# Performance work log

Measured on AMD Instinct MI355X. Metric: run time of the kernel, lower is better.

## Reference

```python
import jax, jax.numpy as jnp
import numpy as np

B, N, D = 1, 4096, 320
HEADS, DIM_HEAD = 8, 40
PHASE, Hm, Wm = 3, 64, 64  # guidance mask spatial dims; Hm*Wm == N


def setup_inputs() -> dict:
    key = jax.random.key(0)
    ks = jax.random.split(key, 7)
    s = 0.02
    x = jax.random.normal(ks[0], (B, N, D), jnp.float32)
    guidance_mask = jax.random.bernoulli(ks[1], 0.25, (B, PHASE, Hm, Wm)).astype(jnp.float32)
    Wq = jax.random.normal(ks[2], (D, HEADS * DIM_HEAD), jnp.float32) * s
    Wk = jax.random.normal(ks[3], (D, HEADS * DIM_HEAD), jnp.float32) * s
    Wv = jax.random.normal(ks[4], (D, HEADS * DIM_HEAD), jnp.float32) * s
    Wo = jax.random.normal(ks[5], (HEADS * DIM_HEAD, D), jnp.float32) * s
    bo = jnp.zeros((D,), jnp.float32)
    return {"x": x, "guidance_mask": guidance_mask, "Wq": Wq, "Wk": Wk,
            "Wv": Wv, "Wo": Wo, "bo": bo}


def reference(x, guidance_mask, Wq, Wk, Wv, Wo, bo):
    b, n, _ = x.shape
    h, dh = HEADS, DIM_HEAD
    scale = dh ** (-0.5)

    def split_heads(t):
        # b n (h d) -> (b h) n d
        return t.reshape(b, n, h, dh).transpose(0, 2, 1, 3).reshape(b * h, n, dh)

    q = split_heads(x @ Wq)
    k = split_heads(x @ Wk)
    v = split_heads(x @ Wv)

    sim = jnp.einsum('bid,bjd->bij', q, k) * scale  # (b*h, n, n)

    _, p, Hh, Ww = guidance_mask.shape
    HW = Hh * Ww  # == n
    g = guidance_mask.reshape(b, p, HW)
    # sum over phases of outer products, clamped at 1 (binary block mask)
    mask_sim = jnp.minimum(jnp.einsum('bpi,bpj->bij', g, g), 1.0)  # (b, HW, HW)
    mask_sim = jnp.repeat(mask_sim, h, axis=0)  # (b*h, HW, HW), heads within each b

    neg = -jnp.finfo(sim.dtype).max
    # original: sim[:, :, :HW][mask_sim == 0] = -max ; here n == HW so full matrix
    sim = jnp.where(mask_sim == 0, neg, sim)

    attn = jax.nn.softmax(sim, axis=-1)
    out = jnp.einsum('bij,bjd->bid', attn, v)  # (b*h, n, dh)
    out = out.reshape(b, h, n, dh).transpose(0, 2, 1, 3).reshape(b, n, h * dh)
    return out @ Wo + bo
```

## Files before the change

### kernel.cpp

```cpp
#include <hip/hip_runtime.h>
#include <hip/hip_bf16.h>
#include <stdint.h>

#define NT 4096
#define DM 320
#define NH 8
#define DH 40
#define QSCALE 0.22811013f
#define PSTR 68
#define KFJB 640

typedef float f32x4 __attribute__((ext_vector_type(4)));
typedef __bf16 bf16x8 __attribute__((ext_vector_type(8)));

__device__ __forceinline__ unsigned short f2b(float f) {
  unsigned u = __builtin_bit_cast(unsigned, f);
  u += 0x7FFFu + ((u >> 16) & 1u);
  return (unsigned short)(u >> 16);
}

__device__ __forceinline__ bf16x8 ld_bf8(const unsigned short* p) {
  uint4 v = *(const uint4*)p;
  return __builtin_bit_cast(bf16x8, v);
}

__device__ __forceinline__ f32x4 mfma16(bf16x8 a, bf16x8 b, f32x4 c) {
  return __builtin_amdgcn_mfma_f32_16x16x32_bf16(a, b, c, 0, 0, 0);
}

__device__ __forceinline__ float fexp2(float x) {
#if __has_builtin(__builtin_amdgcn_exp2f)
  return __builtin_amdgcn_exp2f(x);
#else
  float r; asm("v_exp_f32 %0, %1" : "=v"(r) : "v"(x)); return r;
#endif
}

__device__ __forceinline__ uint2 pack4(float a, float b, float c, float d) {
  uint2 pk;
  pk.x = (unsigned)f2b(a) | ((unsigned)f2b(b) << 16);
  pk.y = (unsigned)f2b(c) | ((unsigned)f2b(d) << 16);
  return pk;
}

__device__ __forceinline__ uint4 idfrag(int idx) {
  uint4 r;
  r.x = (idx == 0 ? 0x3F80u : 0u) | (idx == 1 ? 0x3F800000u : 0u);
  r.y = (idx == 2 ? 0x3F80u : 0u) | (idx == 3 ? 0x3F800000u : 0u);
  r.z = (idx == 4 ? 0x3F80u : 0u) | (idx == 5 ? 0x3F800000u : 0u);
  r.w = (idx == 6 ? 0x3F80u : 0u) | (idx == 7 ? 0x3F800000u : 0u);
  return r;
}

__device__ __forceinline__ size_t fmi(int tile, int nk, int k, int o) {
  return ((size_t)tile * nk + (k >> 5)) * 512 + (size_t)((k >> 3) & 3) * 128 +
         (size_t)(o & 15) * 8 + (k & 7);
}

__global__ __launch_bounds__(256) void prep_kernel(
    const float* __restrict__ x, const float* __restrict__ g,
    const float* __restrict__ Wq, const float* __restrict__ Wk,
    const float* __restrict__ Wv, const float* __restrict__ Wo,
    unsigned short* __restrict__ xbf, unsigned char* __restrict__ sgp,
    unsigned short* __restrict__ Wtf, int* __restrict__ perm,
    int* __restrict__ invp, int* __restrict__ nqp,
    unsigned char* __restrict__ tsig) {
  const int b = blockIdx.x, t = threadIdx.x;
  if (b == 100) {
    __shared__ unsigned long long sa[256], sb[256];
    unsigned char mys[16];
    unsigned long long ca = 0ull, cb = 0ull;
#pragma unroll
    for (int i = 0; i < 16; ++i) {
      int tok = t * 16 + i;
      unsigned s = 0;
      if (g[tok] != 0.f)          s |= 1u;
      if (g[NT + tok] != 0.f)     s |= 2u;
      if (g[2 * NT + tok] != 0.f) s |= 4u;
      mys[i] = (unsigned char)s;
      if (s < 4) ca += 1ull << (16 * s);
      else       cb += 1ull << (16 * (s - 4));
    }
    sa[t] = ca; sb[t] = cb;
    __syncthreads();
    for (int off = 1; off < 256; off <<= 1) {
      unsigned long long va = (t >= off) ? sa[t - off] : 0ull;
      unsigned long long vb = (t >= off) ? sb[t - off] : 0ull;
      __syncthreads();
      sa[t] += va; sb[t] += vb;
      __syncthreads();
    }
    const unsigned long long ta = sa[255], tb = sb[255];
    const int t1 = (int)((ta >> 16) & 0xffff), t2 = (int)((ta >> 32) & 0xffff),
              t3 = (int)((ta >> 48) & 0xffff), t4 = (int)(tb & 0xffff),
              t5 = (int)((tb >> 16) & 0xffff), t6 = (int)((tb >> 32) & 0xffff),
              t7 = (int)((tb >> 48) & 0xffff);
    const int b1 = 0, b2 = t1, b3 = b2 + t2, b4 = b3 + t3, b5 = b4 + t4,
              b6 = b5 + t5, b7 = b6 + t6, b0 = b7 + t7;
    unsigned long long ra = sa[t] - ca;
    unsigned long long rb = sb[t] - cb;
    ra += ((unsigned long long)(unsigned)b0)        |
          ((unsigned long long)(unsigned)b1 << 16)  |
          ((unsigned long long)(unsigned)b2 << 32)  |
          ((unsigned long long)(unsigned)b3 << 48);
    rb += ((unsigned long long)(unsigned)b4)        |
          ((unsigned long long)(unsigned)b5 << 16)  |
          ((unsigned long long)(unsigned)b6 << 32)  |
          ((unsigned long long)(unsigned)b7 << 48);
#pragma unroll
    for (int i = 0; i < 16; ++i) {
      int tok = t * 16 + i;
      unsigned s = mys[i];
      int sh = 16 * (int)(s & 3u);
      int p;
      if (s < 4) { p = (int)((ra >> sh) & 0xffff); ra += 1ull << sh; }
      else       { p = (int)((rb >> sh) & 0xffff); rb += 1ull << sh; }
      perm[p] = tok; invp[tok] = p; sgp[p] = (unsigned char)s;
    }
    if (t == 0) nqp[0] = b0;
    if (t < 64) {
      const int lo = t * 64, hi = lo + 64;
      unsigned o = 0;
      if (b1 < hi && b2 > lo && b2 > b1) o |= 1u;
      if (b2 < hi && b3 > lo && b3 > b2) o |= 2u;
      if (b3 < hi && b4 > lo && b4 > b3) o |= 3u;
      if (b4 < hi && b5 > lo && b5 > b4) o |= 4u;
      if (b5 < hi && b6 > lo && b6 > b5) o |= 5u;
      if (b6 < hi && b7 > lo && b7 > b6) o |= 6u;
      if (b7 < hi && b0 > lo && b0 > b7) o |= 7u;
      tsig[t] = (unsigned char)o;
    }
    return;
  }
  if (b > 100) {
    int base = (b - 101) * 2560;
#pragma unroll
    for (int j = 0; j < 10; ++j) {
      int i = (base + j * 256 + t) * 4;
      int m = i / DM, k = i % DM;
      float4 v = *(const float4*)(x + i);
      ushort4 u;
      u.x = f2b(v.x); u.y = f2b(v.y); u.z = f2b(v.z); u.w = f2b(v.w);
      *(ushort4*)(xbf + fmi(m >> 4, 10, k, m)) = u;
    }
    return;
  }
  __shared__ __align__(16) unsigned short lt[64 * 72];
  int kx = b % 5, cy = b / 5;
  int cm = cy % 5;
  const float* src;
  int rowbase;
  if (cy < 5)       { src = Wq; rowbase = cm * 64; }
  else if (cy < 10) { src = Wk; rowbase = 320 + cm * 64; }
  else if (cy < 15) { src = Wv; rowbase = 640 + cm * 64; }
  else              { src = Wo; rowbase = 960 + cm * 64; }
  const int c0 = cm * 64;
  const int k0 = kx * 64;
#pragma unroll
  for (int i = 0; i < 4; ++i) {
    int kr = (t >> 4) + i * 16, cc = (t & 15) * 4;
    float4 w4 = *(const float4*)&src[(size_t)(k0 + kr) * DM + c0 + cc];
    lt[(cc + 0) * 72 + kr] = f2b(w4.x);
    lt[(cc + 1) * 72 + kr] = f2b(w4.y);
    lt[(cc + 2) * 72 + kr] = f2b(w4.z);
    lt[(cc + 3) * 72 + kr] = f2b(w4.w);
  }
  __syncthreads();
#pragma unroll
  for (int i = 0; i < 2; ++i) {
    int idx = t + i * 256, cl = idx >> 3, ch = idx & 7;
    int c = rowbase + cl, k = k0 + ch * 8;
    *(uint4*)&Wtf[fmi(c >> 4, 10, k, c)] = *(const uint4*)&lt[cl * 72 + ch * 8];
  }
}

__global__ __launch_bounds__(256, 4) void qkv_gemm(
    const unsigned short* __restrict__ xbf, const unsigned short* __restrict__ Wtf,
    const int* __restrict__ invp,
    unsigned short* __restrict__ Qb, unsigned short* __restrict__ Kf,
    unsigned short* __restrict__ Vk) {
  const int t = threadIdx.x;
  const int w = t >> 6, lane = t & 63, quad = lane >> 4, ln = lane & 15;
  const int m0 = blockIdx.x * 64;
  const int cy = blockIdx.y;
  const int a = cy / 5;
  const int cc0 = (cy % 5) * 64;
  const int mt = (m0 >> 4) + w;
  const int ct0 = a * 20 + (cc0 >> 4);

  f32x4 acc[4] = {{0,0,0,0},{0,0,0,0},{0,0,0,0},{0,0,0,0}};
  for (int kc = 0; kc < 10; ++kc) {
    bf16x8 xf = ld_bf8(xbf + ((size_t)(mt * 10 + kc)) * 512 + lane * 8);
#pragma unroll
    for (int nt = 0; nt < 4; ++nt) {
      bf16x8 wf = ld_bf8(Wtf + ((size_t)((ct0 + nt) * 10 + kc)) * 512 + lane * 8);
      acc[nt] = mfma16(wf, xf, acc[nt]);
    }
  }
  const int bp = invp[m0 + w * 16 + ln];
  if (a == 0) {
#pragma unroll
    for (int nt = 0; nt < 4; ++nt) {
      int c = cc0 + nt * 16 + quad * 4;
      int h = c / DH, d = c % DH;
      uint2 pk = pack4(acc[nt][0] * QSCALE, acc[nt][1] * QSCALE,
                       acc[nt][2] * QSCALE, acc[nt][3] * QSCALE);
      *(uint2*)&Qb[((size_t)h * NT + bp) * 64 + d] = pk;
    }
  } else {
    unsigned short* dst = (a == 1) ? Kf : Vk;
#pragma unroll
    for (int nt = 0; nt < 4; ++nt) {
      int c = cc0 + nt * 16 + quad * 4;
      int h = c / DH, d = c % DH;
      uint2 pk = pack4(acc[nt][0], acc[nt][1], acc[nt][2], acc[nt][3]);
      size_t base = ((size_t)h * 256 + (bp >> 4)) * KFJB;
      size_t idx = (d < 32)
          ? base + (size_t)(d >> 3) * 128 + (size_t)(bp & 15) * 8 + (d & 7)
          : base + 512 + (size_t)(bp & 15) * 8 + (d - 32);
      *(uint2*)&dst[idx] = pk;
    }
  }
}

__global__ __launch_bounds__(256) void retile_kernel(
    const unsigned short* __restrict__ Vk, unsigned short* __restrict__ Vf) {
  const int t = threadIdx.x;
  const int w = t >> 6, lane = t & 63, ln = lane & 15, jg = lane >> 4;
  const bf16x8 b1f = __builtin_bit_cast(bf16x8, idfrag(ln - jg * 8));
  const bf16x8 b2f = __builtin_bit_cast(bf16x8, idfrag(ln + 16 - jg * 8));
  const uint4 z4 = {0, 0, 0, 0};
#pragma unroll
  for (int i = 0; i < 4; ++i) {
    const int task = (blockIdx.x * 4 + w) * 4 + i;
    const int h = task >> 8, jb = task & 255;
    const unsigned short* kb = Vk + ((size_t)h * 256 + jb) * KFJB;
    uint4 f0 = *(const uint4*)(kb + lane * 8);
    uint4 f1 = z4;
    if (lane < 16) f1 = *(const uint4*)(kb + 512 + lane * 8);
    f32x4 d1 = {0,0,0,0}, d2 = {0,0,0,0}, d3 = {0,0,0,0};
    d1 = mfma16(__builtin_bit_cast(bf16x8, f0), b1f, d1);
    d2 = mfma16(__builtin_bit_cast(bf16x8, f0), b2f, d2);
    d3 = mfma16(__builtin_bit_cast(bf16x8, f1), b1f, d3);
    const int bp = jb * 16 + jg * 4;
#pragma unroll
    for (int ot = 0; ot < 3; ++ot) {
      int dd = ot * 16 + ln;
      if (ot == 2 && ln >= 8) continue;
      f32x4 dv = (ot == 0) ? d1 : (ot == 1) ? d2 : d3;
      size_t idx = ((((((size_t)(h * 64 + (bp >> 6)) * 3 + (dd >> 4)) * 2 +
                       ((bp >> 5) & 1)) * 4 + ((bp >> 3) & 3)) * 16 + (dd & 15))) * 8 +
                   (bp & 7);
      *(uint2*)&Vf[idx] = pack4(dv[0], dv[1], dv[2], dv[3]);
    }
  }
}

__global__ __launch_bounds__(256, 4) void attn_kernel(
    const unsigned short* __restrict__ Qb, const unsigned short* __restrict__ Kf,
    const unsigned short* __restrict__ Vf, const unsigned char* __restrict__ sgp,
    const int* __restrict__ perm, const int* __restrict__ nqp,
    const unsigned char* __restrict__ tsg,
    unsigned short* __restrict__ Abf, unsigned short* __restrict__ Ubf) {
  __shared__ __align__(16) unsigned short pt[4][16 * PSTR];
  __shared__ float red[3][12][64];
  __shared__ float vs[4][48];
  __shared__ __align__(16) unsigned short ob[16][40];
  const int t = threadIdx.x;
  const int w = t >> 6, lane = t & 63, quad = lane >> 4, ln = lane & 15;
  const int h = blockIdx.y;
  const int nq = nqp[0];
  const int nkt = (nq + 63) >> 6;
  const int nq_pad = (nq + 127) & ~127;

  const unsigned short* Vfh = Vf + (size_t)h * 196608;
  const uint4 z4 = {0, 0, 0, 0};
  const uint4 ones4 = {0x3F803F80u, 0x3F803F80u, 0x3F803F80u, 0x3F803F80u};
  const bf16x8 onesb = __builtin_bit_cast(bf16x8, ones4);

  if (blockIdx.x == 256) {
    f32x4 o[3] = {{0,0,0,0},{0,0,0,0},{0,0,0,0}};
    for (int jt = w; jt < 64; jt += 4) {
#pragma unroll
      for (int ot = 0; ot < 3; ++ot) {
        uint4 v0 = *(const uint4*)(Vfh + ((size_t)((jt * 3 + ot) * 2 + 0)) * 512 +
                                   lane * 8);
        uint4 v1 = *(const uint4*)(Vfh + ((size_t)((jt * 3 + ot) * 2 + 1)) * 512 +
                                   lane * 8);
        o[ot] = mfma16(__builtin_bit_cast(bf16x8, v0), onesb, o[ot]);
        o[ot] = mfma16(__builtin_bit_cast(bf16x8, v1), onesb, o[ot]);
      }
    }
    if (ln == 0) {
#pragma unroll
      for (int ot = 0; ot < 3; ++ot)
#pragma unroll
        for (int r = 0; r < 4; ++r) vs[w][ot * 16 + quad * 4 + r] = o[ot][r];
    }
    __syncthreads();
    if (t < DH) {
      float s = vs[0][t] + vs[1][t] + vs[2][t] + vs[3][t];
      Ubf[h * DH + t] = f2b(s * (1.0f / (float)NT));
    }
    return;
  }

  const int qrow = blockIdx.x * 16;
  if (qrow >= nq_pad) return;

  unsigned qv = *(const unsigned*)(sgp + qrow)     | *(const unsigned*)(sgp + qrow + 4)
              | *(const unsigned*)(sgp + qrow + 8) | *(const unsigned*)(sgp + qrow + 12);
  qv |= qv >> 16; qv |= qv >> 8;
  const unsigned qor = qv & 255u;

  const unsigned short* Kfh = Kf + (size_t)h * 256 * KFJB;
  unsigned short* ptw = pt[w];
  const bool vone = (ln == 8);

  bf16x8 qa[2];
  unsigned sqx4;
  f32x4 o[3] = {{0,0,0,0},{0,0,0,0},{0,0,0,0}};

  {
    int bp = qrow + ln;
    const unsigned short* Qp = Qb + ((size_t)h * NT + bp) * 64;
    qa[0] = ld_bf8(Qp + quad * 8);
    uint4 q1 = z4;
    if (quad == 0) q1 = *(const uint4*)(Qp + 32);
    qa[1] = __builtin_bit_cast(bf16x8, q1);
    sqx4 = (unsigned)sgp[bp] * 0x01010101u;
  }

  for (int jt = w; jt < nkt; jt += 4) {
    if ((tsg[jt] & qor) == 0) continue;
    uint4 kfr0[4], kfr1[4];
#pragma unroll
    for (int nt = 0; nt < 4; ++nt) {
      const unsigned short* kb = Kfh + (size_t)(jt * 4 + nt) * KFJB;
      kfr0[nt] = *(const uint4*)(kb + lane * 8);
      kfr1[nt] = z4;
      if (lane < 16) kfr1[nt] = *(const uint4*)(kb + 512 + lane * 8);
    }
#pragma unroll
    for (int nt = 0; nt < 4; ++nt) {
      bf16x8 ka0 = __builtin_bit_cast(bf16x8, kfr0[nt]);
      bf16x8 ka1 = __builtin_bit_cast(bf16x8, kfr1[nt]);
      unsigned spj = *(const unsigned*)(sgp + jt * 64 + nt * 16 + quad * 4);
      f32x4 acc = {0.f, 0.f, 0.f, 0.f};
      acc = mfma16(ka0, qa[0], acc);
      acc = mfma16(ka1, qa[1], acc);
      unsigned m4 = spj & sqx4;
      unsigned u[4];
#pragma unroll
      for (int r = 0; r < 4; ++r) {
        unsigned mb = (m4 >> (8 * r)) & 255u;
        float am = mb ? acc[r] : -3.0e38f;
        u[r] = __builtin_bit_cast(unsigned, fexp2(am));
      }
      uint2 pk;
      pk.x = (u[0] >> 16) | (u[1] & 0xffff0000u);
      pk.y = (u[2] >> 16) | (u[3] & 0xffff0000u);
      *(uint2*)&ptw[ln * PSTR + nt * 16 + quad * 4] = pk;
    }
    uint4 vfr[6];
#pragma unroll
    for (int ot = 0; ot < 3; ++ot)
#pragma unroll
      for (int c = 0; c < 2; ++c)
        vfr[ot * 2 + c] =
            *(const uint4*)(Vfh + ((size_t)((jt * 3 + ot) * 2 + c)) * 512 + lane * 8);
    if (vone) { vfr[4] = ones4; vfr[5] = ones4; }

    bf16x8 pb[2];
    asm volatile("s_waitcnt lgkmcnt(0)" ::: "memory");
    pb[0] = ld_bf8(&ptw[ln * PSTR + quad * 8]);
    pb[1] = ld_bf8(&ptw[ln * PSTR + 32 + quad * 8]);
#pragma unroll
    for (int ot = 0; ot < 3; ++ot) {
      bf16x8 va0 = __builtin_bit_cast(bf16x8, vfr[ot * 2]);
      bf16x8 va1 = __builtin_bit_cast(bf16x8, vfr[ot * 2 + 1]);
      o[ot] = mfma16(va0, pb[0], o[ot]);
      o[ot] = mfma16(va1, pb[1], o[ot]);
    }
  }

  if (w) {
#pragma unroll
    for (int ot = 0; ot < 3; ++ot)
#pragma unroll
      for (int r = 0; r < 4; ++r)
        red[w - 1][ot * 4 + r][lane] = o[ot][r];
  }
  __syncthreads();
  if (w == 0) {
#pragma unroll
    for (int ot = 0; ot < 3; ++ot)
#pragma unroll
      for (int r = 0; r < 4; ++r) {
        float s = o[ot][r];
        s += red[0][ot * 4 + r][lane];
        s += red[1][ot * 4 + r][lane];
        s += red[2][ot * 4 + r][lane];
        o[ot][r] = s;
      }
    float Lb = __shfl(o[2][0], 32 + ln, 64);
    float inv = 1.f / Lb;
#pragma unroll
    for (int ot = 0; ot < 3; ++ot) {
      int d0 = ot * 16 + quad * 4;
      if (d0 < DH) {
        uint2 pk = pack4(o[ot][0] * inv, o[ot][1] * inv,
                         o[ot][2] * inv, o[ot][3] * inv);
        *(uint2*)&ob[ln][d0] = pk;
      }
    }
    asm volatile("s_waitcnt lgkmcnt(0)" ::: "memory");
#pragma unroll
    for (int p = 0; p < 2; ++p) {
      int idx = p * 64 + lane;
      if (idx < 80) {
        int row = idx / 5, cc = idx % 5;
        int m = perm[qrow + row];
        uint4 vv = *(const uint4*)&ob[row][cc * 8];
        *(uint4*)&Abf[fmi(m >> 4, 10, h * DH + cc * 8, m)] = vv;
      }
    }
  }
}

__global__ __launch_bounds__(256, 4) void out_gemm(
    const unsigned short* __restrict__ Abf, const unsigned short* __restrict__ Wtf,
    const float* __restrict__ bo, const int* __restrict__ invp,
    const int* __restrict__ nqp, const unsigned short* __restrict__ Ubf,
    float* __restrict__ out) {
  const int t = threadIdx.x;
  const int w = t >> 6, lane = t & 63, quad = lane >> 4, ln = lane & 15;
  const int m0 = blockIdx.x * 32;
  const int cc0 = blockIdx.y * 64;
  const int mt = (m0 >> 4) + (w >> 1);
  const int m = m0 + (w >> 1) * 16 + ln;
  const int nb = (w & 1) * 2;
  const int ct0 = 60 + (cc0 >> 4) + nb;
  const bool uni = invp[m] >= nqp[0];

  f32x4 acc[2] = {{0,0,0,0},{0,0,0,0}};
  for (int kc = 0; kc < 10; ++kc) {
    uint4 uv = *(const uint4*)(Ubf + kc * 32 + quad * 8);
    uint4 av = *(const uint4*)(Abf + ((size_t)(mt * 10 + kc)) * 512 + lane * 8);
    if (uni) av = uv;
    bf16x8 af = __builtin_bit_cast(bf16x8, av);
#pragma unroll
    for (int nt = 0; nt < 2; ++nt) {
      bf16x8 wf = ld_bf8(Wtf + ((size_t)((ct0 + nt) * 10 + kc)) * 512 + lane * 8);
      acc[nt] = mfma16(wf, af, acc[nt]);
    }
  }
#pragma unroll
  for (int nt = 0; nt < 2; ++nt) {
    int c = cc0 + (nb + nt) * 16 + quad * 4;
    float4 bv = *(const float4*)(bo + c);
    float4 ov;
    ov.x = acc[nt][0] + bv.x;
    ov.y = acc[nt][1] + bv.y;
    ov.z = acc[nt][2] + bv.z;
    ov.w = acc[nt][3] + bv.w;
    *(float4*)(out + (size_t)m * DM + c) = ov;
  }
}

extern "C" void kernel_launch(void* const* d_in, const int* in_sizes, int n_in,
                              void* d_out, int out_size, void* d_ws, size_t ws_size,
                              hipStream_t stream) {
  const float* x  = (const float*)d_in[0];
  const float* g  = (const float*)d_in[1];
  const float* Wq = (const float*)d_in[2];
  const float* Wk = (const float*)d_in[3];
  const float* Wv = (const float*)d_in[4];
  const float* Wo = (const float*)d_in[5];
  const float* bo = (const float*)d_in[6];
  float* out = (float*)d_out;

  char* ws = (char*)d_ws;
  const size_t SGP_OFF  = 0;
  const size_t NQ_OFF   = 4096;
  const size_t TSIG_OFF = 4224;
  const size_t PERM_OFF = 8192;
  const size_t INV_OFF  = 24576;
  const size_t XBF_OFF  = 40960;
  const size_t WTF_OFF = XBF_OFF + (size_t)NT * DM * 2;
  const size_t QB_OFF  = WTF_OFF + (size_t)1280 * DM * 2;
  const size_t KF_OFF  = QB_OFF + (size_t)NH * NT * 64 * 2;
  const size_t VK_OFF  = KF_OFF + (size_t)NH * 256 * KFJB * 2;
  const size_t VF_OFF  = VK_OFF + (size_t)NH * 256 * KFJB * 2;
  const size_t UBF_OFF = VF_OFF + (size_t)NH * 196608 * 2;
  const size_t ABF_OFF = UBF_OFF + 4096;
  unsigned char* sgp   = (unsigned char*)(ws + SGP_OFF);
  int* nqp             = (int*)(ws + NQ_OFF);
  unsigned char* tsig  = (unsigned char*)(ws + TSIG_OFF);
  int* perm            = (int*)(ws + PERM_OFF);
  int* invp            = (int*)(ws + INV_OFF);
  unsigned short* xbf  = (unsigned short*)(ws + XBF_OFF);
  unsigned short* Wtf  = (unsigned short*)(ws + WTF_OFF);
  unsigned short* Qb   = (unsigned short*)(ws + QB_OFF);
  unsigned short* Kf   = (unsigned short*)(ws + KF_OFF);
  unsigned short* Vk   = (unsigned short*)(ws + VK_OFF);
  unsigned short* Vf   = (unsigned short*)(ws + VF_OFF);
  unsigned short* Ubf  = (unsigned short*)(ws + UBF_OFF);
  unsigned short* Abf  = (unsigned short*)(ws + ABF_OFF);

  prep_kernel<<<229, 256, 0, stream>>>(x, g, Wq, Wk, Wv, Wo, xbf, sgp, Wtf,
                                       perm, invp, nqp, tsig);
  qkv_gemm<<<dim3(64, 15), 256, 0, stream>>>(xbf, Wtf, invp, Qb, Kf, Vk);
  retile_kernel<<<128, 256, 0, stream>>>(Vk, Vf);
  attn_kernel<<<dim3(257, NH), 256, 0, stream>>>(Qb, Kf, Vf, sgp, perm, nqp,
                                                 tsig, Abf, Ubf);
  out_gemm<<<dim3(128, 5), 256, 0, stream>>>(Abf, Wtf, bo, invp, nqp, Ubf, out);
}
```

Baseline: 123.6 us.

## Compact active key tiles per wave and prefetch next tile's K fragments

Each wave now builds a compacted list of key tiles that survive the guidance-mask test, using a ballot and popcount stored in shared memory, so the loop no longer branches over skipped tiles. Within the loop, half of the next tile's K fragments are loaded early and V loads are issued before the QK MFMAs. This is meant to hide global load latency behind compute. It costs extra registers for the prefetched fragments, which may lower occupancy under the launch bounds of 4 blocks.

New measurement: 126.3 us. 1.02x slower.

```diff
diff --git a/kernel.cpp b/kernel.cpp
--- a/kernel.cpp
+++ b/kernel.cpp
@@ -266,6 +266,7 @@
   __shared__ float red[3][12][64];
   __shared__ float vs[4][48];
   __shared__ __align__(16) unsigned short ob[16][40];
+  __shared__ unsigned char kl[4][16];
   const int t = threadIdx.x;
   const int w = t >> 6, lane = t & 63, quad = lane >> 4, ln = lane & 15;
   const int h = blockIdx.y;
@@ -313,6 +314,17 @@
   qv |= qv >> 16; qv |= qv >> 8;
   const unsigned qor = qv & 255u;
 
+  int nk2;
+  {
+    int cand = w + lane * 4;
+    bool keep = (lane < 16) && (cand < nkt) && ((tsg[cand] & qor) != 0u);
+    unsigned long long mk = __ballot(keep);
+    nk2 = __popcll(mk);
+    if (keep)
+      kl[w][__popcll(mk & ((1ull << lane) - 1ull))] = (unsigned char)cand;
+  }
+  asm volatile("s_waitcnt lgkmcnt(0)" ::: "memory");
+
   const unsigned short* Kfh = Kf + (size_t)h * 256 * KFJB;
   unsigned short* ptw = pt[w];
   const bool vone = (ln == 8);
@@ -331,20 +343,52 @@
     sqx4 = (unsigned)sgp[bp] * 0x01010101u;
   }
 
-  for (int jt = w; jt < nkt; jt += 4) {
-    if ((tsg[jt] & qor) == 0) continue;
-    uint4 kfr0[4], kfr1[4];
+  uint4 kc0[2], kc1[2];
+  if (nk2 > 0) {
+    const int j0 = kl[w][0];
+#pragma unroll
+    for (int nt = 0; nt < 2; ++nt) {
+      const unsigned short* kb = Kfh + (size_t)(j0 * 4 + nt) * KFJB;
+      kc0[nt] = *(const uint4*)(kb + lane * 8);
+      kc1[nt] = z4;
+      if (lane < 16) kc1[nt] = *(const uint4*)(kb + 512 + lane * 8);
+    }
+  }
+
+  for (int i = 0; i < nk2; ++i) {
+    const int jt = kl[w][i];
+    uint4 kh0[2], kh1[2];
+#pragma unroll
+    for (int nt = 0; nt < 2; ++nt) {
+      const unsigned short* kb = Kfh + (size_t)(jt * 4 + 2 + nt) * KFJB;
+      kh0[nt] = *(const uint4*)(kb + lane * 8);
+      kh1[nt] = z4;
+      if (lane < 16) kh1[nt] = *(const uint4*)(kb + 512 + lane * 8);
+    }
+    uint4 vfr[6];
+#pragma unroll
+    for (int ot = 0; ot < 3; ++ot)
+#pragma unroll
+      for (int c = 0; c < 2; ++c)
+        vfr[ot * 2 + c] =
+            *(const uint4*)(Vfh + ((size_t)((jt * 3 + ot) * 2 + c)) * 512 + lane * 8);
+    if (vone) { vfr[4] = ones4; vfr[5] = ones4; }
+    uint4 kn0[2], kn1[2];
+    const bool hasnext = (i + 1 < nk2);
+    if (hasnext) {
+      const int jn = kl[w][i + 1];
+#pragma unroll
+      for (int nt = 0; nt < 2; ++nt) {
+        const unsigned short* kb = Kfh + (size_t)(jn * 4 + nt) * KFJB;
+        kn0[nt] = *(const uint4*)(kb + lane * 8);
+        kn1[nt] = z4;
+        if (lane < 16) kn1[nt] = *(const uint4*)(kb + 512 + lane * 8);
+      }
+    }
 #pragma unroll
     for (int nt = 0; nt < 4; ++nt) {
-      const unsigned short* kb = Kfh + (size_t)(jt * 4 + nt) * KFJB;
-      kfr0[nt] = *(const uint4*)(kb + lane * 8);
-      kfr1[nt] = z4;
-      if (lane < 16) kfr1[nt] = *(const uint4*)(kb + 512 + lane * 8);
-    }
-#pragma unroll
-    for (int nt = 0; nt < 4; ++nt) {
-      bf16x8 ka0 = __builtin_bit_cast(bf16x8, kfr0[nt]);
-      bf16x8 ka1 = __builtin_bit_cast(bf16x8, kfr1[nt]);
+      bf16x8 ka0 = __builtin_bit_cast(bf16x8, nt < 2 ? kc0[nt] : kh0[nt - 2]);
+      bf16x8 ka1 = __builtin_bit_cast(bf16x8, nt < 2 ? kc1[nt] : kh1[nt - 2]);
       unsigned spj = *(const unsigned*)(sgp + jt * 64 + nt * 16 + quad * 4);
       f32x4 acc = {0.f, 0.f, 0.f, 0.f};
       acc = mfma16(ka0, qa[0], acc);
@@ -362,14 +406,6 @@
       pk.y = (u[2] >> 16) | (u[3] & 0xffff0000u);
       *(uint2*)&ptw[ln * PSTR + nt * 16 + quad * 4] = pk;
     }
-    uint4 vfr[6];
-#pragma unroll
-    for (int ot = 0; ot < 3; ++ot)
-#pragma unroll
-      for (int c = 0; c < 2; ++c)
-        vfr[ot * 2 + c] =
-            *(const uint4*)(Vfh + ((size_t)((jt * 3 + ot) * 2 + c)) * 512 + lane * 8);
-    if (vone) { vfr[4] = ones4; vfr[5] = ones4; }
 
     bf16x8 pb[2];
     asm volatile("s_waitcnt lgkmcnt(0)" ::: "memory");
@@ -381,6 +417,10 @@
       bf16x8 va1 = __builtin_bit_cast(bf16x8, vfr[ot * 2 + 1]);
       o[ot] = mfma16(va0, pb[0], o[ot]);
       o[ot] = mfma16(va1, pb[1], o[ot]);
+    }
+    if (hasnext) {
+      kc0[0] = kn0[0]; kc0[1] = kn0[1];
+      kc1[0] = kn1[0]; kc1[1] = kn1[1];
     }
   }
 
```
